# Kernel optimization log

Measured on AMD Instinct MI355X. Metric: run time of the kernel, lower is better.

## Reference

```python
import jax, jax.numpy as jnp
import numpy as np

N, P, C, M = 64, 8732, 91, 20          # batch, n_priors (SSD300), n_classes, padded objects/image
THRESHOLD = 0.5
NEG_POS_RATIO = 3
ALPHA = 1.0


def setup_inputs() -> dict:
    key = jax.random.key(0)
    k = jax.random.split(key, 7)
    predicted_locs = jax.random.normal(k[0], (N, P, 4), jnp.float32)
    predicted_scores = jax.random.normal(k[1], (N, P, C), jnp.float32)
    # ground-truth boxes in boundary (x1,y1,x2,y2) format, valid fractional coords
    xy = jax.random.uniform(k[2], (N, M, 2), minval=0.0, maxval=0.6)
    wh = jax.random.uniform(k[3], (N, M, 2), minval=0.05, maxval=0.4)
    boxes = jnp.concatenate([xy, xy + wh], axis=-1)
    labels = jax.random.randint(k[4], (N, M), 1, C).astype(jnp.int32)  # 0 = background
    # prior boxes in center-size (cx,cy,w,h) format
    cxy = jax.random.uniform(k[5], (P, 2), minval=0.05, maxval=0.95)
    pwh = jax.random.uniform(k[6], (P, 2), minval=0.05, maxval=0.3)
    priors_cxcy = jnp.concatenate([cxy, pwh], axis=-1)
    return dict(predicted_locs=predicted_locs, predicted_scores=predicted_scores,
                boxes=boxes, labels=labels, priors_cxcy=priors_cxcy)


def _iou(a, b):
    # a: (M,4) xyxy, b: (P,4) xyxy -> (M,P)
    lo = jnp.maximum(a[:, None, :2], b[None, :, :2])
    hi = jnp.minimum(a[:, None, 2:], b[None, :, 2:])
    inter = jnp.clip(hi - lo, 0.0).prod(-1)
    area_a = (a[:, 2:] - a[:, :2]).prod(-1)
    area_b = (b[:, 2:] - b[:, :2]).prod(-1)
    return inter / (area_a[:, None] + area_b[None, :] - inter)


def _xy_to_cxcy(xy):
    return jnp.concatenate([(xy[..., :2] + xy[..., 2:]) * 0.5, xy[..., 2:] - xy[..., :2]], -1)


def _cxcy_to_gcxgcy(cxcy, priors):
    g_cxcy = (cxcy[..., :2] - priors[..., :2]) / (priors[..., 2:] / 10.0)
    g_wh = jnp.log(cxcy[..., 2:] / priors[..., 2:]) * 5.0
    return jnp.concatenate([g_cxcy, g_wh], -1)


def _match_one(boxes_i, labels_i, priors_cxcy, priors_xy):
    overlap = _iou(boxes_i, priors_xy)                    # (M, P)
    ov_per_prior = overlap.max(0)                         # (P,)
    obj_per_prior = overlap.argmax(0)                     # (P,)
    prior_per_obj = overlap.argmax(1)                     # (M,)
    # force each object onto its best prior with overlap 1
    obj_per_prior = obj_per_prior.at[prior_per_obj].set(jnp.arange(M))
    ov_per_prior = ov_per_prior.at[prior_per_obj].set(1.0)
    label_per_prior = labels_i[obj_per_prior]             # (P,)
    label_per_prior = jnp.where(ov_per_prior < THRESHOLD, 0, label_per_prior)
    true_locs = _cxcy_to_gcxgcy(_xy_to_cxcy(boxes_i[obj_per_prior]), priors_cxcy)  # (P,4)
    return label_per_prior, true_locs


def reference(predicted_locs, predicted_scores, boxes, labels, priors_cxcy):
    priors_xy = jnp.concatenate([priors_cxcy[:, :2] - priors_cxcy[:, 2:] * 0.5,
                                 priors_cxcy[:, :2] + priors_cxcy[:, 2:] * 0.5], -1)
    true_classes, true_locs = jax.vmap(_match_one, in_axes=(0, 0, None, None))(
        boxes, labels, priors_cxcy, priors_xy)            # (N,P), (N,P,4)

    pos = true_classes != 0                               # (N, P)
    n_pos = pos.sum(1)                                    # (N,)
    n_pos_total = n_pos.sum().astype(jnp.float32)

    # localization: smooth L1 (beta=1), mean over positive elements
    d = predicted_locs - true_locs
    sl1 = jnp.where(jnp.abs(d) < 1.0, 0.5 * d * d, jnp.abs(d) - 0.5)   # (N,P,4)
    loc_loss = (sl1 * pos[..., None]).sum() / (n_pos_total * 4.0)

    # confidence: per-prior cross entropy
    logp = jax.nn.log_softmax(predicted_scores, axis=-1)  # (N,P,C)
    ce = -jnp.take_along_axis(logp, true_classes[..., None], axis=-1)[..., 0]  # (N,P)

    conf_loss_pos = (ce * pos).sum()
    # hard negative mining: sort negative losses desc, take 3*n_pos per image
    ce_neg = jnp.where(pos, 0.0, ce)
    ce_neg_sorted = jnp.sort(ce_neg, axis=1)[:, ::-1]     # (N,P) descending
    hard_neg = jnp.arange(P)[None, :] < (NEG_POS_RATIO * n_pos)[:, None]
    conf_loss_hard_neg = (ce_neg_sorted * hard_neg).sum()

    conf_loss = (conf_loss_pos + conf_loss_hard_neg) / n_pos_total
    return conf_loss + ALPHA * loc_loss
```

## Files before the change

kernel.cpp:

```cpp
#include <hip/hip_runtime.h>

#define NN 64
#define PP 8732
#define CC 91
#define MM 20
#define RATIO 3
#define BPI 8
#define CHUNK 1092
#define ROWS 128
#define BTHR 512
#define TILES2 ((NN * PP) / ROWS)

typedef unsigned long long u64;
typedef unsigned short u16;

__global__ __launch_bounds__(256) void match_a(
    const float4* __restrict__ boxes4,
    const float4* __restrict__ priors4,
    const int* __restrict__ labels,
    u16* __restrict__ minfo,
    u64* __restrict__ combined_part,
    int* __restrict__ counter)
{
  __shared__ float bx0[MM], by0[MM], bx1[MM], by1[MM], ba[MM];
  __shared__ int lb[MM];
  __shared__ u64 wkey[4][MM];
  const int blk = blockIdx.x, tid = threadIdx.x;
  const int wave = tid >> 6, lane = tid & 63;
  const int n = blk >> 3, part = blk & 7;
  const int c0 = part * CHUNK;
  const int cend = (c0 + CHUNK < PP) ? c0 + CHUNK : PP;

  if (blk == 0 && tid == 0) counter[0] = 0;

  if (tid < MM) {
    float4 b = boxes4[n * MM + tid];
    bx0[tid] = b.x; by0[tid] = b.y; bx1[tid] = b.z; by1[tid] = b.w;
    ba[tid] = (b.z - b.x) * (b.w - b.y);
    lb[tid] = labels[n * MM + tid];
  }
  __syncthreads();

  float bi[MM], bd[MM]; int bpp[MM];
#pragma unroll
  for (int m = 0; m < MM; ++m) { bi[m] = 0.0f; bd[m] = 1.0f; bpp[m] = 0; }

#pragma unroll
  for (int i = 0; i < 5; ++i) {
    int p = c0 + tid + i * 256;
    if (p < cend) {
      float4 pr = priors4[p];
      float hw = pr.z * 0.5f, hh = pr.w * 0.5f;
      float px0 = pr.x - hw, py0 = pr.y - hh, px1 = pr.x + hw, py1 = pr.y + hh;
      float pa = (px1 - px0) * (py1 - py0);
      float pi = -1.0f, pd = 1.0f; int pm = 0;
#pragma unroll
      for (int m = 0; m < MM; ++m) {
        float iw = fminf(bx1[m], px1) - fmaxf(bx0[m], px0);
        float ih = fminf(by1[m], py1) - fmaxf(by0[m], py0);
        iw = fmaxf(iw, 0.0f); ih = fmaxf(ih, 0.0f);
        float inter = iw * ih;
        float den = (ba[m] + pa) - inter;
        bool c1 = inter * pd > pi * den;
        pi = c1 ? inter : pi; pd = c1 ? den : pd; pm = c1 ? m : pm;
        bool c2 = inter * bd[m] > bi[m] * den;
        bi[m] = c2 ? inter : bi[m]; bd[m] = c2 ? den : bd[m];
        bpp[m] = c2 ? p : bpp[m];
      }
      float q = pi / pd;
      int lab8 = (q < 0.5f) ? 0 : lb[pm];
      minfo[(size_t)n * PP + p] = (u16)((pm << 8) | lab8);
    }
  }

#pragma unroll
  for (int m = 0; m < MM; ++m) {
    float r = bi[m] / bd[m];
    u64 key = ((u64)__float_as_uint(r) << 32) | (unsigned)(~(unsigned)bpp[m]);
#pragma unroll
    for (int d = 1; d < 64; d <<= 1) {
      u64 o = __shfl_xor(key, d);
      key = (o > key) ? o : key;
    }
    if (lane == 0) wkey[wave][m] = key;
  }
  __syncthreads();
  if (tid < MM) {
    u64 best = wkey[0][tid];
    u64 o1 = wkey[1][tid], o2 = wkey[2][tid], o3 = wkey[3][tid];
    best = (o1 > best) ? o1 : best;
    best = (o2 > best) ? o2 : best;
    best = (o3 > best) ? o3 : best;
    combined_part[blk * MM + tid] = best;
  }
}

__global__ __launch_bounds__(BTHR) void ce_kernel(
    const float* __restrict__ scores,
    const float4* __restrict__ pred_locs4,
    const float4* __restrict__ priors4,
    const float4* __restrict__ boxes4,
    const int* __restrict__ labels,
    const u16* __restrict__ minfo,
    const u64* __restrict__ combined_part,
    float* __restrict__ ce_neg,
    float4* __restrict__ partials)
{
  __shared__ unsigned key_lo[2][MM];
  __shared__ int lbl_s[2][MM];
  __shared__ float4 box_s[2][MM];
  __shared__ float4 w8[8];
  const int tid = threadIdx.x;
  const long base = (long)blockIdx.x * ROWS;
  const int n0 = (int)(base / PP);
  const int rem0 = (int)(base - (long)n0 * PP);
  const int r = tid >> 2, l = tid & 3;
  const long row = base + r;

  const int mi = minfo[row];

  if (tid < MM) {
    const u64* cp = combined_part + (size_t)n0 * BPI * MM;
    u64 best = cp[tid];
#pragma unroll
    for (int w = 1; w < BPI; ++w) { u64 o = cp[w * MM + tid]; best = (o > best) ? o : best; }
    key_lo[0][tid] = (unsigned)best;
    lbl_s[0][tid]  = labels[n0 * MM + tid];
    box_s[0][tid]  = boxes4[n0 * MM + tid];
  } else if (tid >= 64 && tid < 64 + MM) {
    int j = tid - 64, nn = (n0 + 1 < NN) ? n0 + 1 : NN - 1;
    const u64* cp = combined_part + (size_t)nn * BPI * MM;
    u64 best = cp[j];
#pragma unroll
    for (int w = 1; w < BPI; ++w) { u64 o = cp[w * MM + j]; best = (o > best) ? o : best; }
    key_lo[1][j] = (unsigned)best;
    lbl_s[1][j]  = labels[nn * MM + j];
    box_s[1][j]  = boxes4[nn * MM + j];
  }

  const float* rp = scores + (size_t)row * CC;
  float ss0 = 0.f, ss1 = 0.f, ss2 = 0.f, ss3 = 0.f;
#pragma unroll
  for (int j = 0; j < 23; ++j) {
    int c = l + 4 * j;
    if (c < CC) {
      float e = __expf(rp[c]);
      if ((j & 3) == 0) ss0 += e;
      else if ((j & 3) == 1) ss1 += e;
      else if ((j & 3) == 2) ss2 += e;
      else ss3 += e;
    }
  }
  float s = (ss0 + ss1) + (ss2 + ss3);
  s += __shfl_xor(s, 1);
  s += __shfl_xor(s, 2);

  __syncthreads();

  float cp_ = 0.0f, lp_ = 0.0f; int pos0 = 0, pos1 = 0;
  if (l == 0) {
    const int bn = (rem0 + r >= PP) ? 1 : 0;
    const int p = rem0 + r - bn * PP;
    int mm_ = -1;
    const unsigned want = ~(unsigned)p;
#pragma unroll
    for (int j = 0; j < MM; ++j) if (key_lo[bn][j] == want) mm_ = j;
    bool pos; int lab, sm;
    if (mm_ >= 0) { pos = true; sm = mm_; lab = lbl_s[bn][mm_]; }
    else { lab = mi & 0xff; pos = (lab != 0); sm = mi >> 8; }
    float ce = __logf(s) - rp[lab];
    if (pos) {
      cp_ = ce; ce_neg[row] = 0.0f;
      if (bn) pos1 = 1; else pos0 = 1;
      float4 bx = box_s[bn][sm], pr = priors4[p], pl = pred_locs4[row];
      float cx = (bx.x + bx.z) * 0.5f, cy = (bx.y + bx.w) * 0.5f;
      float w = bx.z - bx.x, h = bx.w - bx.y;
      float gx = (cx - pr.x) / (pr.z / 10.0f);
      float gy = (cy - pr.y) / (pr.w / 10.0f);
      float gz = __logf(w / pr.z) * 5.0f;
      float gw = __logf(h / pr.w) * 5.0f;
      float d, a;
      d = pl.x - gx; a = fabsf(d); lp_ += (a < 1.0f) ? 0.5f * d * d : a - 0.5f;
      d = pl.y - gy; a = fabsf(d); lp_ += (a < 1.0f) ? 0.5f * d * d : a - 0.5f;
      d = pl.z - gz; a = fabsf(d); lp_ += (a < 1.0f) ? 0.5f * d * d : a - 0.5f;
      d = pl.w - gw; a = fabsf(d); lp_ += (a < 1.0f) ? 0.5f * d * d : a - 0.5f;
    } else {
      ce_neg[row] = fmaxf(ce, 0.0f);
    }
  }

#pragma unroll
  for (int d = 1; d < 64; d <<= 1) {
    cp_ += __shfl_xor(cp_, d); lp_ += __shfl_xor(lp_, d);
    pos0 += __shfl_xor(pos0, d); pos1 += __shfl_xor(pos1, d);
  }
  if ((tid & 63) == 0)
    w8[tid >> 6] = make_float4(cp_, lp_, (float)pos0, (float)pos1);
  __syncthreads();
  if (tid == 0) {
    float sx = 0.f, sy = 0.f, sz = 0.f, sw = 0.f;
#pragma unroll
    for (int w = 0; w < 8; ++w) { sx += w8[w].x; sy += w8[w].y; sz += w8[w].z; sw += w8[w].w; }
    partials[blockIdx.x] = make_float4(sx, sy, sz, sw);
  }
}

__global__ __launch_bounds__(256) void hardneg_kernel(
    const float* __restrict__ ce_neg, const float4* __restrict__ partials,
    float4* __restrict__ per_img, int* __restrict__ counter,
    float* __restrict__ out)
{
  __shared__ int4 cred[2][4];
  __shared__ float wredf[4];
  __shared__ int wcnt[4];
  __shared__ float4 wacc[4];
  __shared__ int last_s;
  const int n = blockIdx.x, tid = threadIdx.x;

  unsigned uv[35];
#pragma unroll
  for (int i = 0; i < 35; ++i) {
    int p = tid + (i << 8);
    uv[i] = (p < PP) ? __float_as_uint(ce_neg[(size_t)n * PP + p]) : 0u;
  }

  float kc = 0.0f, cpo = 0.0f, lpo = 0.0f;
  {
    const int bstart = (n * PP) / ROWS;
    const int bend = ((n + 1) * PP - 1) / ROWS;
    const int ost = (n * PP + ROWS - 1) / ROWS;
    const int oen = ((n + 1) * PP + ROWS - 1) / ROWS;
    for (int b = bstart + tid; b <= bend; b += 256) {
      float4 pb = partials[b];
      int nb0 = (b * ROWS) / PP;
      if (nb0 == n)     kc += pb.z;
      if (nb0 + 1 == n) kc += pb.w;
      if (b >= ost && b < oen) { cpo += pb.x; lpo += pb.y; }
    }
#pragma unroll
    for (int d = 1; d < 64; d <<= 1) {
      kc += __shfl_xor(kc, d); cpo += __shfl_xor(cpo, d); lpo += __shfl_xor(lpo, d);
    }
    if ((tid & 63) == 0) wacc[tid >> 6] = make_float4(kc, cpo, lpo, 0.f);
    __syncthreads();
    kc = wacc[0].x + wacc[1].x + wacc[2].x + wacc[3].x;
    cpo = wacc[0].y + wacc[1].y + wacc[2].y + wacc[3].y;
    lpo = wacc[0].z + wacc[1].z + wacc[2].z + wacc[3].z;
  }
  const float npn = kc;
  const int k = RATIO * (int)(kc + 0.5f);

  float hs = 0.0f;
  if (k >= PP) {
    float s = 0.0f;
#pragma unroll
    for (int i = 0; i < 35; ++i) s += __uint_as_float(uv[i]);
#pragma unroll
    for (int d = 1; d < 64; d <<= 1) s += __shfl_xor(s, d);
    __syncthreads();
    if ((tid & 63) == 0) wredf[tid >> 6] = s;
    __syncthreads();
    hs = wredf[0] + wredf[1] + wredf[2] + wredf[3];
  } else if (k > 0) {
    unsigned lo = 0u, hi = 0x7f7fffffu;
    int it = 0;
    while (lo < hi) {
      unsigned span = hi - lo;
      unsigned q4 = span >> 2;
      unsigned m1, m2, m3;
      if (q4 == 0) { m1 = m2 = m3 = lo + ((span + 1) >> 1); }
      else { m1 = lo + q4; m2 = lo + 2 * q4; m3 = lo + 3 * q4; }
      int a1 = 0, a2 = 0, a3 = 0;
#pragma unroll
      for (int i = 0; i < 35; ++i) {
        unsigned v = uv[i];
        a1 += (v >= m1); a2 += (v >= m2); a3 += (v >= m3);
      }
#pragma unroll
      for (int d = 1; d < 64; d <<= 1) {
        a1 += __shfl_xor(a1, d); a2 += __shfl_xor(a2, d); a3 += __shfl_xor(a3, d);
      }
      const int buf = it & 1;
      if ((tid & 63) == 0) cred[buf][tid >> 6] = make_int4(a1, a2, a3, 0);
      __syncthreads();
      int c1 = 0, c2 = 0, c3 = 0;
#pragma unroll
      for (int w = 0; w < 4; ++w) {
        int4 cc = cred[buf][w];
        c1 += cc.x; c2 += cc.y; c3 += cc.z;
      }
      if (c3 >= k) lo = m3;
      else if (c2 >= k) { lo = m2; hi = m3 - 1; }
      else if (c1 >= k) { lo = m1; hi = m2 - 1; }
      else hi = m1 - 1;
      ++it;
    }
    const float x = __uint_as_float(lo);
    float s = 0.0f; int c = 0;
#pragma unroll
    for (int i = 0; i < 35; ++i) {
      unsigned v = uv[i];
      if (v > lo) { s += __uint_as_float(v); ++c; }
    }
#pragma unroll
    for (int d = 1; d < 64; d <<= 1) { s += __shfl_xor(s, d); c += __shfl_xor(c, d); }
    __syncthreads();
    if ((tid & 63) == 0) { wredf[tid >> 6] = s; wcnt[tid >> 6] = c; }
    __syncthreads();
    hs = (wredf[0] + wredf[1] + wredf[2] + wredf[3]) +
         (float)(k - (wcnt[0] + wcnt[1] + wcnt[2] + wcnt[3])) * x;
  }

  if (tid == 0) {
    per_img[n] = make_float4(cpo, lpo, npn, hs);
    __threadfence();
    last_s = atomicAdd(counter, 1);
  }
  __syncthreads();
  if (last_s == NN - 1) {
    __threadfence();
    if (tid < 64) {
      float4 v = per_img[tid];
      float a = v.x, b = v.y, c = v.z, d = v.w;
#pragma unroll
      for (int dd = 1; dd < 64; dd <<= 1) {
        a += __shfl_xor(a, dd); b += __shfl_xor(b, dd);
        c += __shfl_xor(c, dd); d += __shfl_xor(d, dd);
      }
      if (tid == 0) out[0] = (a + d) / c + b / (c * 4.0f);
    }
  }
}

extern "C" void kernel_launch(void* const* d_in, const int* in_sizes, int n_in,
                              void* d_out, int out_size, void* d_ws, size_t ws_size,
                              hipStream_t stream) {
  const float*  pred_locs   = (const float*)d_in[0];
  const float*  pred_scores = (const float*)d_in[1];
  const float*  boxes       = (const float*)d_in[2];
  const int*    labels      = (const int*)d_in[3];
  const float*  priors      = (const float*)d_in[4];
  float* out = (float*)d_out;

  u16* minfo = (u16*)d_ws;
  float4* partials = (float4*)(minfo + (size_t)NN * PP);
  float*  ce_neg = (float*)(partials + TILES2);
  u64* combined_part = (u64*)(ce_neg + (size_t)NN * PP);
  float4* per_img = (float4*)(combined_part + NN * BPI * MM);
  int* counter = (int*)(per_img + NN);

  match_a<<<NN * BPI, 256, 0, stream>>>((const float4*)boxes,
                                        (const float4*)priors, labels,
                                        minfo, combined_part, counter);
  ce_kernel<<<TILES2, BTHR, 0, stream>>>(pred_scores, (const float4*)pred_locs,
                                         (const float4*)priors,
                                         (const float4*)boxes, labels,
                                         minfo, combined_part,
                                         ce_neg, partials);
  hardneg_kernel<<<NN, 256, 0, stream>>>(ce_neg, partials, per_img, counter, out);
}
```

Before: 83.75 us.

## Split matching kernel objects across waves and use more, smaller prior chunks

The prior-object matching kernel now runs 32 blocks per image instead of 8, with chunks of 273 priors. Each of the 4 waves handles 5 of the 20 ground-truth objects for all priors in the chunk, rather than every thread looping over all 20 objects. Per-wave best-object candidates go to shared memory and are reduced across waves before the match info is written. Per-object best-prior keys are written per wave, so the later kernel merges 4x more partial entries. This cuts per-thread register and serial work and raises block count, at the cost of a shared-memory reduction pass and more partial keys to combine.

```diff
diff --git a/kernel.cpp b/kernel.cpp
--- a/kernel.cpp
+++ b/kernel.cpp
@@ -5,8 +5,8 @@
 #define CC 91
 #define MM 20
 #define RATIO 3
-#define BPI 8
-#define CHUNK 1092
+#define BPI 32
+#define CHUNK 273
 #define ROWS 128
 #define BTHR 512
 #define TILES2 ((NN * PP) / ROWS)
@@ -14,7 +14,7 @@
 typedef unsigned long long u64;
 typedef unsigned short u16;
 
-__global__ __launch_bounds__(256) void match_a(
+__global__ __launch_bounds__(256) void match_b(
     const float4* __restrict__ boxes4,
     const float4* __restrict__ priors4,
     const int* __restrict__ labels,
@@ -22,76 +22,85 @@
     u64* __restrict__ combined_part,
     int* __restrict__ counter)
 {
-  __shared__ float bx0[MM], by0[MM], bx1[MM], by1[MM], ba[MM];
+  __shared__ float pi_s[4][CHUNK];
+  __shared__ float pd_s[4][CHUNK];
+  __shared__ short pm_s[4][CHUNK];
   __shared__ int lb[MM];
-  __shared__ u64 wkey[4][MM];
   const int blk = blockIdx.x, tid = threadIdx.x;
   const int wave = tid >> 6, lane = tid & 63;
-  const int n = blk >> 3, part = blk & 7;
+  const int n = blk >> 5, part = blk & 31;
   const int c0 = part * CHUNK;
   const int cend = (c0 + CHUNK < PP) ? c0 + CHUNK : PP;
-
-  if (blk == 0 && tid == 0) counter[0] = 0;
-
-  if (tid < MM) {
-    float4 b = boxes4[n * MM + tid];
-    bx0[tid] = b.x; by0[tid] = b.y; bx1[tid] = b.z; by1[tid] = b.w;
-    ba[tid] = (b.z - b.x) * (b.w - b.y);
-    lb[tid] = labels[n * MM + tid];
-  }
-  __syncthreads();
-
-  float bi[MM], bd[MM]; int bpp[MM];
-#pragma unroll
-  for (int m = 0; m < MM; ++m) { bi[m] = 0.0f; bd[m] = 1.0f; bpp[m] = 0; }
+  const int clen = cend - c0;
+
+  if (blockIdx.x == 0 && tid == 0) counter[0] = 0;
+  if (tid < MM) lb[tid] = labels[n * MM + tid];
+
+  float obx0[5], oby0[5], obx1[5], oby1[5], oba[5];
+#pragma unroll
+  for (int j = 0; j < 5; ++j) {
+    float4 b = boxes4[n * MM + wave * 5 + j];
+    obx0[j] = b.x; oby0[j] = b.y; obx1[j] = b.z; oby1[j] = b.w;
+    oba[j] = (b.z - b.x) * (b.w - b.y);
+  }
+
+  float bi[5], bd[5]; int bpp[5];
+#pragma unroll
+  for (int j = 0; j < 5; ++j) { bi[j] = 0.0f; bd[j] = 1.0f; bpp[j] = 0; }
 
 #pragma unroll
   for (int i = 0; i < 5; ++i) {
-    int p = c0 + tid + i * 256;
-    if (p < cend) {
+    int pc = lane + (i << 6);
+    if (pc < clen) {
+      int p = c0 + pc;
       float4 pr = priors4[p];
       float hw = pr.z * 0.5f, hh = pr.w * 0.5f;
       float px0 = pr.x - hw, py0 = pr.y - hh, px1 = pr.x + hw, py1 = pr.y + hh;
       float pa = (px1 - px0) * (py1 - py0);
       float pi = -1.0f, pd = 1.0f; int pm = 0;
 #pragma unroll
-      for (int m = 0; m < MM; ++m) {
-        float iw = fminf(bx1[m], px1) - fmaxf(bx0[m], px0);
-        float ih = fminf(by1[m], py1) - fmaxf(by0[m], py0);
+      for (int j = 0; j < 5; ++j) {
+        float iw = fminf(obx1[j], px1) - fmaxf(obx0[j], px0);
+        float ih = fminf(oby1[j], py1) - fmaxf(oby0[j], py0);
         iw = fmaxf(iw, 0.0f); ih = fmaxf(ih, 0.0f);
         float inter = iw * ih;
-        float den = (ba[m] + pa) - inter;
-        bool c1 = inter * pd > pi * den;
-        pi = c1 ? inter : pi; pd = c1 ? den : pd; pm = c1 ? m : pm;
-        bool c2 = inter * bd[m] > bi[m] * den;
-        bi[m] = c2 ? inter : bi[m]; bd[m] = c2 ? den : bd[m];
-        bpp[m] = c2 ? p : bpp[m];
-      }
-      float q = pi / pd;
-      int lab8 = (q < 0.5f) ? 0 : lb[pm];
-      minfo[(size_t)n * PP + p] = (u16)((pm << 8) | lab8);
-    }
-  }
-
-#pragma unroll
-  for (int m = 0; m < MM; ++m) {
-    float r = bi[m] / bd[m];
-    u64 key = ((u64)__float_as_uint(r) << 32) | (unsigned)(~(unsigned)bpp[m]);
+        float den = (oba[j] + pa) - inter;
+        bool cA = inter * pd > pi * den;
+        pi = cA ? inter : pi; pd = cA ? den : pd;
+        pm = cA ? (wave * 5 + j) : pm;
+        bool cB = inter * bd[j] > bi[j] * den;
+        bi[j] = cB ? inter : bi[j]; bd[j] = cB ? den : bd[j];
+        bpp[j] = cB ? p : bpp[j];
+      }
+      pi_s[wave][pc] = pi; pd_s[wave][pc] = pd; pm_s[wave][pc] = (short)pm;
+    }
+  }
+
+#pragma unroll
+  for (int j = 0; j < 5; ++j) {
+    float r = bi[j] / bd[j];
+    u64 key = ((u64)__float_as_uint(r) << 32) | (unsigned)(~(unsigned)bpp[j]);
 #pragma unroll
     for (int d = 1; d < 64; d <<= 1) {
       u64 o = __shfl_xor(key, d);
       key = (o > key) ? o : key;
     }
-    if (lane == 0) wkey[wave][m] = key;
+    if (lane == 0) combined_part[blk * MM + wave * 5 + j] = key;
   }
   __syncthreads();
-  if (tid < MM) {
-    u64 best = wkey[0][tid];
-    u64 o1 = wkey[1][tid], o2 = wkey[2][tid], o3 = wkey[3][tid];
-    best = (o1 > best) ? o1 : best;
-    best = (o2 > best) ? o2 : best;
-    best = (o3 > best) ? o3 : best;
-    combined_part[blk * MM + tid] = best;
+
+  for (int pc = tid; pc < clen; pc += 256) {
+    float pi = pi_s[0][pc], pd = pd_s[0][pc]; int pm = pm_s[0][pc];
+#pragma unroll
+    for (int w = 1; w < 4; ++w) {
+      float qi = pi_s[w][pc], qd = pd_s[w][pc];
+      bool c = qi * pd > pi * qd;
+      int qm = pm_s[w][pc];
+      pi = c ? qi : pi; pd = c ? qd : pd; pm = c ? qm : pm;
+    }
+    float q = pi / pd;
+    int lab8 = (q < 0.5f) ? 0 : lb[pm];
+    minfo[(size_t)n * PP + c0 + pc] = (u16)((pm << 8) | lab8);
   }
 }
 
@@ -346,16 +355,18 @@
   float4* partials = (float4*)(minfo + (size_t)NN * PP);
   float*  ce_neg = (float*)(partials + TILES2);
   u64* combined_part = (u64*)(ce_neg + (size_t)NN * PP);
-  float4* per_img = (float4*)(combined_part + NN * BPI * MM);
+  float4* per_img = (float4*)(combined_part + (size_t)NN * BPI * MM);
   int* counter = (int*)(per_img + NN);
 
-  match_a<<<NN * BPI, 256, 0, stream>>>((const float4*)boxes,
+  match_b<<<NN * BPI, 256, 0, stream>>>((const float4*)boxes,
                                         (const float4*)priors, labels,
                                         minfo, combined_part, counter);
-  ce_kernel<<<TILES2, BTHR, 0, stream>>>(pred_scores, (const float4*)pred_locs,
+  ce_kernel<<<TILES2, BTHR, 0, stream>>>(pred_scores,
+                                         (const float4*)pred_locs,
                                          (const float4*)priors,
                                          (const float4*)boxes, labels,
                                          minfo, combined_part,
                                          ce_neg, partials);
-  hardneg_kernel<<<NN, 256, 0, stream>>>(ce_neg, partials, per_img, counter, out);
+  hardneg_kernel<<<NN, 256, 0, stream>>>(ce_neg, partials, per_img,
+                                         counter, out);
 }
```

New measurement: 81.68 us. 1.03x faster.
